# Kernel tuning notes

Hardware: AMD Instinct MI355X
Metric: run time of the kernel (lower is better)

The kernel has to match this reference:

```python
import jax, jax.numpy as jnp
import numpy as np

B, N, DIM, DEPTH, H, DH, MLP = 8, 1024, 768, 6, 12, 64, 3072
INNER = H * DH
LN_EPS = 1e-5


def setup_inputs() -> dict:
    key = jax.random.key(0)
    ks = jax.random.split(key, 8)
    return {
        "x": jax.random.normal(ks[0], (B, N, DIM), jnp.float32),
        "ln1_g": jnp.ones((DEPTH, DIM), jnp.float32),
        "ln1_b": jnp.zeros((DEPTH, DIM), jnp.float32),
        "Wq": jax.random.normal(ks[1], (DEPTH, DIM, INNER), jnp.float32) * 0.02,
        "Wkv": jax.random.normal(ks[2], (DEPTH, DIM, 2 * INNER), jnp.float32) * 0.02,
        "mix_pre": jax.random.normal(ks[3], (DEPTH, H, H), jnp.float32),
        "mix_post": jax.random.normal(ks[4], (DEPTH, H, H), jnp.float32),
        "Wo": jax.random.normal(ks[5], (DEPTH, INNER, DIM), jnp.float32) * 0.02,
        "bo": jnp.zeros((DEPTH, DIM), jnp.float32),
        "s1": jnp.full((DEPTH, DIM), 0.1, jnp.float32),  # LayerScale init_eps for depth<=18
        "ln2_g": jnp.ones((DEPTH, DIM), jnp.float32),
        "ln2_b": jnp.zeros((DEPTH, DIM), jnp.float32),
        "W1": jax.random.normal(ks[6], (DEPTH, DIM, MLP), jnp.float32) * 0.02,
        "b1": jnp.zeros((DEPTH, MLP), jnp.float32),
        "W2": jax.random.normal(ks[7], (DEPTH, MLP, DIM), jnp.float32) * 0.02,
        "b2": jnp.zeros((DEPTH, DIM), jnp.float32),
        "s2": jnp.full((DEPTH, DIM), 0.1, jnp.float32),
    }


def _ln(x, g, b):
    m = jnp.mean(x, axis=-1, keepdims=True)
    v = jnp.mean(jnp.square(x - m), axis=-1, keepdims=True)
    return (x - m) * jax.lax.rsqrt(v + LN_EPS) * g + b


def reference(x, ln1_g, ln1_b, Wq, Wkv, mix_pre, mix_post, Wo, bo, s1,
              ln2_g, ln2_b, W1, b1, W2, b2, s2):
    depth = Wq.shape[0]
    heads = mix_pre.shape[-1]
    dim_head = Wq.shape[-1] // heads
    scale = dim_head ** -0.5
    b_, n_ = x.shape[0], x.shape[1]

    def split_heads(t):  # [b, n, h*d] -> [b, h, n, d]
        return t.reshape(b_, n_, heads, dim_head).transpose(0, 2, 1, 3)

    for i in range(depth):
        # --- talking-heads attention block (PreNorm + LayerScale) ---
        h = _ln(x, ln1_g[i], ln1_b[i])
        q = split_heads(h @ Wq[i])
        kv = h @ Wkv[i]
        k = split_heads(kv[..., : heads * dim_head])
        v = split_heads(kv[..., heads * dim_head:])
        dots = jnp.einsum('bhid,bhjd->bhij', q, k) * scale
        dots = jnp.einsum('bhij,hg->bgij', dots, mix_pre[i])  # pre-softmax head mix
        attn = jax.nn.softmax(dots, axis=-1)
        attn = jnp.einsum('bhij,hg->bgij', attn, mix_post[i])  # post-softmax head mix
        out = jnp.einsum('bhij,bhjd->bhid', attn, v)
        out = out.transpose(0, 2, 1, 3).reshape(b_, n_, heads * dim_head)
        x = (out @ Wo[i] + bo[i]) * s1[i] + x
        # --- feed-forward block (PreNorm + LayerScale) ---
        h = _ln(x, ln2_g[i], ln2_b[i])
        h = jax.nn.gelu(h @ W1[i] + b1[i], approximate=False) @ W2[i] + b2[i]
        x = h * s2[i] + x
    return x
```

## Files before the change

kernel.cpp:

```cpp
#include <hip/hip_runtime.h>

constexpr int kDepth = 6;
constexpr int kB = 8;
constexpr int kN = 1024;
constexpr int kDim = 768;
constexpr int kH = 12;
constexpr int kDh = 64;
constexpr int kMlp = 3072;
constexpr int kRows = kB * kN;
constexpr int kQKV = 2304;

typedef __attribute__((ext_vector_type(4))) float f32x4;
typedef __attribute__((ext_vector_type(8))) short bf16x8;

__device__ __forceinline__ f32x4 mfma16x16x32(bf16x8 a, bf16x8 b, f32x4 c) {
  return __builtin_amdgcn_mfma_f32_16x16x32_bf16(a, b, c, 0, 0, 0);
}

__device__ __forceinline__ unsigned short f2bf(float f) {
  unsigned int u = __builtin_bit_cast(unsigned int, f);
  u = u + 0x7FFFu + ((u >> 16) & 1u);
  return (unsigned short)(u >> 16);
}

__device__ __forceinline__ float bf2f(unsigned short u) {
  return __builtin_bit_cast(float, (unsigned int)u << 16);
}

__device__ __forceinline__ void gload_lds16(const void* g, void* l) {
  __builtin_amdgcn_global_load_lds((__attribute__((address_space(1))) void*)g,
                                   (__attribute__((address_space(3))) void*)l,
                                   16, 0, 0);
}

__global__ __launch_bounds__(256) void ln_kernel(const float* __restrict__ x,
                                                 const float* __restrict__ gamma,
                                                 const float* __restrict__ beta,
                                                 unsigned short* __restrict__ out) {
  int row = blockIdx.x, tid = threadIdx.x;
  const float* xr = x + (size_t)row * kDim;
  float v0 = xr[tid], v1 = xr[tid + 256], v2 = xr[tid + 512];
  float s = v0 + v1 + v2;
  float q = v0 * v0 + v1 * v1 + v2 * v2;
#pragma unroll
  for (int o = 32; o >= 1; o >>= 1) {
    s += __shfl_xor(s, o);
    q += __shfl_xor(q, o);
  }
  __shared__ float ss[4], sq[4];
  int wid = tid >> 6, lane = tid & 63;
  if (lane == 0) { ss[wid] = s; sq[wid] = q; }
  __syncthreads();
  s = ss[0] + ss[1] + ss[2] + ss[3];
  q = sq[0] + sq[1] + sq[2] + sq[3];
  float mean = s * (1.0f / kDim);
  float var = q * (1.0f / kDim) - mean * mean;
  float rstd = rsqrtf(var + 1e-5f);
  unsigned short* orow = out + (size_t)row * kDim;
  orow[tid]       = f2bf((v0 - mean) * rstd * gamma[tid]       + beta[tid]);
  orow[tid + 256] = f2bf((v1 - mean) * rstd * gamma[tid + 256] + beta[tid + 256]);
  orow[tid + 512] = f2bf((v2 - mean) * rstd * gamma[tid + 512] + beta[tid + 512]);
}

__global__ __launch_bounds__(256) void transpose_all(const float* __restrict__ Wq,
                                                     const float* __restrict__ Wkv,
                                                     const float* __restrict__ Wo,
                                                     const float* __restrict__ W1,
                                                     const float* __restrict__ W2,
                                                     unsigned short* __restrict__ wqkvT,
                                                     unsigned short* __restrict__ woT,
                                                     unsigned short* __restrict__ w1T,
                                                     unsigned short* __restrict__ w2T,
                                                     int L) {
  int t = blockIdx.x;
  const float* src;
  unsigned short* dst;
  int R, C, dstOff;
  if (t < 576)       { src = Wq  + (size_t)L * 768 * 768;  R = 768;  C = 768;  dst = wqkvT; dstOff = 0;   }
  else if (t < 1728) { src = Wkv + (size_t)L * 768 * 1536; R = 768;  C = 1536; dst = wqkvT; dstOff = 768; t -= 576; }
  else if (t < 2304) { src = Wo  + (size_t)L * 768 * 768;  R = 768;  C = 768;  dst = woT;   dstOff = 0;   t -= 1728; }
  else if (t < 4608) { src = W1  + (size_t)L * 768 * 3072; R = 768;  C = 3072; dst = w1T;   dstOff = 0;   t -= 2304; }
  else               { src = W2  + (size_t)L * 3072 * 768; R = 3072; C = 768;  dst = w2T;   dstOff = 0;   t -= 4608; }
  int Ct = C >> 5;
  int bx = t % Ct, by = t / Ct;
  __shared__ float tt[32][33];
  int tx = threadIdx.x & 31, ty = threadIdx.x >> 5;
  int c0 = bx * 32, r0 = by * 32;
#pragma unroll
  for (int k = 0; k < 4; ++k) {
    int r = r0 + ty + k * 8;
    tt[ty + k * 8][tx] = src[(size_t)r * C + c0 + tx];
  }
  __syncthreads();
#pragma unroll
  for (int k = 0; k < 4; ++k) {
    int c = c0 + ty + k * 8;
    dst[(size_t)(dstOff + c) * R + r0 + tx] = f2bf(tt[tx][ty + k * 8]);
  }
}

__global__ __launch_bounds__(256) void transpose_v_kernel(const unsigned short* __restrict__ qkv,
                                                          unsigned short* __restrict__ vT) {
  __shared__ unsigned short t[32][33];
  int tx = threadIdx.x & 31, ty = threadIdx.x >> 5;
  int j0 = blockIdx.x * 32, d0 = blockIdx.y * 32;
  int bg = blockIdx.z;
  int b = bg / kH, g = bg % kH;
#pragma unroll
  for (int k = 0; k < 4; ++k) {
    int j = j0 + ty + k * 8;
    t[ty + k * 8][tx] = qkv[(size_t)(b * kN + j) * kQKV + 1536 + g * 64 + d0 + tx];
  }
  __syncthreads();
#pragma unroll
  for (int k = 0; k < 4; ++k) {
    int d = d0 + ty + k * 8;
    vT[((size_t)(b * kH + g) * kDh + d) * kN + j0 + tx] = t[tx][ty + k * 8];
  }
}

template <int EPI>
__global__ __launch_bounds__(256) void gemm_kernel(const unsigned short* __restrict__ A,
                                                   const unsigned short* __restrict__ Bt,
                                                   const float* __restrict__ bias,
                                                   const float* __restrict__ scl,
                                                   float* __restrict__ resid,
                                                   unsigned short* __restrict__ C,
                                                   int K, int ldc) {
  __shared__ __align__(16) unsigned short lA[128 * 64];
  __shared__ __align__(16) unsigned short lB[128 * 64];
  int tid = threadIdx.x, wid = tid >> 6, lane = tid & 63;
  int gx = gridDim.x;
  int nwg = gx * gridDim.y;
  int orig = blockIdx.y * gx + blockIdx.x;
  int chunk = nwg >> 3;
  int wg = (orig & 7) * chunk + (orig >> 3);
  int bx = wg % gx, by = wg / gx;
  int row0 = by * 128, col0 = bx * 128;
  int wr = wid >> 1, wc = wid & 1;
  f32x4 zero = {0.f, 0.f, 0.f, 0.f};
  f32x4 acc[4][4];
#pragma unroll
  for (int m = 0; m < 4; ++m)
#pragma unroll
    for (int n = 0; n < 4; ++n) acc[m][n] = zero;

  for (int kt = 0; kt < K; kt += 64) {
    __syncthreads();
#pragma unroll
    for (int t = 0; t < 4; ++t) {
      int cbase = wid * 256 + t * 64;
      int c = cbase + lane;
      int r = c >> 3, slot = c & 7;
      int k8 = slot ^ (r & 7);
      gload_lds16(&A[(size_t)(row0 + r) * K + kt + k8 * 8], &lA[cbase * 8]);
      gload_lds16(&Bt[(size_t)(col0 + r) * K + kt + k8 * 8], &lB[cbase * 8]);
    }
    __syncthreads();
#pragma unroll
    for (int kk = 0; kk < 2; ++kk) {
      bf16x8 af[4], bfr[4];
      int kslot = kk * 4 + (lane >> 4);
#pragma unroll
      for (int m = 0; m < 4; ++m) {
        int r = wr * 64 + m * 16 + (lane & 15);
        af[m] = *reinterpret_cast<const bf16x8*>(&lA[r * 64 + ((kslot ^ (r & 7)) << 3)]);
      }
#pragma unroll
      for (int n = 0; n < 4; ++n) {
        int r = wc * 64 + n * 16 + (lane & 15);
        bfr[n] = *reinterpret_cast<const bf16x8*>(&lB[r * 64 + ((kslot ^ (r & 7)) << 3)]);
      }
#pragma unroll
      for (int m = 0; m < 4; ++m)
#pragma unroll
        for (int n = 0; n < 4; ++n) acc[m][n] = mfma16x16x32(af[m], bfr[n], acc[m][n]);
    }
  }
#pragma unroll
  for (int m = 0; m < 4; ++m)
#pragma unroll
    for (int n = 0; n < 4; ++n)
#pragma unroll
      for (int r4 = 0; r4 < 4; ++r4) {
        int row = row0 + wr * 64 + m * 16 + ((lane >> 4) << 2) + r4;
        int col = col0 + wc * 64 + n * 16 + (lane & 15);
        float v = acc[m][n][r4];
        if (EPI == 0) {
          C[(size_t)row * ldc + col] = f2bf(v);
        } else if (EPI == 1) {
          v += bias[col];
          v = 0.5f * v * (1.f + erff(v * 0.70710678118654752f));
          C[(size_t)row * ldc + col] = f2bf(v);
        } else {
          v = (v + bias[col]) * scl[col];
          size_t idx = (size_t)row * kDim + col;
          resid[idx] = resid[idx] + v;
        }
      }
}

__global__ __launch_bounds__(256) void dots_kernel(const unsigned short* __restrict__ qkv,
                                                   unsigned short* __restrict__ dots,
                                                   int i0, int IC) {
  constexpr int TROW = 24;
  __shared__ __align__(16) unsigned short T[32 * 32 * TROW];
  int tid = threadIdx.x, wid = tid >> 6, lane = tid & 63;
  int kg = lane >> 4, l15 = lane & 15;
  int j0 = blockIdx.x * 32;
  int il0 = blockIdx.y * 32;
  int b = blockIdx.z;
  for (int idx = tid; idx < 2048; idx += 256) {
    int pos = idx >> 1;
    *(unsigned int*)&T[pos * TROW + 12 + (idx & 1) * 2] = 0u;
  }
  f32x4 zero = {0.f, 0.f, 0.f, 0.f};
#pragma unroll
  for (int rep = 0; rep < 3; ++rep) {
    int h = rep * 4 + wid;
    f32x4 acc[2][2];
    acc[0][0] = zero; acc[0][1] = zero; acc[1][0] = zero; acc[1][1] = zero;
#pragma unroll
    for (int kk = 0; kk < 2; ++kk) {
      bf16x8 aq[2], bk[2];
#pragma unroll
      for (int m = 0; m < 2; ++m) {
        int tok = i0 + il0 + m * 16 + l15;
        aq[m] = *reinterpret_cast<const bf16x8*>(
            &qkv[(size_t)(b * kN + tok) * kQKV + h * 64 + kk * 32 + kg * 8]);
      }
#pragma unroll
      for (int n = 0; n < 2; ++n) {
        int tj = j0 + n * 16 + l15;
        bk[n] = *reinterpret_cast<const bf16x8*>(
            &qkv[(size_t)(b * kN + tj) * kQKV + 768 + h * 64 + kk * 32 + kg * 8]);
      }
#pragma unroll
      for (int m = 0; m < 2; ++m)
#pragma unroll
        for (int n = 0; n < 2; ++n) acc[m][n] = mfma16x16x32(aq[m], bk[n], acc[m][n]);
    }
#pragma unroll
    for (int m = 0; m < 2; ++m)
#pragma unroll
      for (int n = 0; n < 2; ++n)
#pragma unroll
        for (int r = 0; r < 4; ++r)
          T[((m * 16 + kg * 4 + r) * 32 + n * 16 + l15) * TROW + h] = f2bf(acc[m][n][r]);
  }
  __syncthreads();
#pragma unroll
  for (int k = 0; k < 8; ++k) {
    int c = tid + k * 256;
    int pos = c >> 1, half = c & 1;
    int ii = pos >> 5, jj = pos & 31;
    *(f32x4*)&dots[((size_t)(b * IC + il0 + ii) * kN + j0 + jj) * 16 + half * 8] =
        *(const f32x4*)&T[pos * TROW + half * 8];
  }
}

__global__ __launch_bounds__(256) void softmax_mix_kernel(const unsigned short* __restrict__ dots,
                                                          const float* __restrict__ pre,
                                                          const float* __restrict__ post,
                                                          unsigned short* __restrict__ pbuf,
                                                          int IC) {
  constexpr int EROW = 24;
  __shared__ __align__(16) unsigned short E[1024 * EROW];
  __shared__ __align__(16) unsigned short preA[16 * 32];
  __shared__ __align__(16) unsigned short postA[16 * 32];
  __shared__ float red[4][16];
  __shared__ float lgs[16];
  int tid = threadIdx.x, wid = tid >> 6, lane = tid & 63;
  int kg = lane >> 4, l15 = lane & 15;
  int i = blockIdx.x, b = blockIdx.y;
  for (int idx = tid; idx < 512; idx += 256) {
    int m = idx >> 5, k = idx & 31;
    preA[idx] = f2bf((m < 12 && k < 12) ? pre[k * 12 + m] * 0.125f : 0.f);
  }
  __syncthreads();
  bf16x8 preF = *(const bf16x8*)&preA[l15 * 32 + kg * 8];
  const unsigned short* drow = dots + (size_t)(b * IC + i) * kN * 16;
  f32x4 zero = {0.f, 0.f, 0.f, 0.f};
  bf16x8 zfrag = {0, 0, 0, 0, 0, 0, 0, 0};
  float psum[4] = {0.f, 0.f, 0.f, 0.f};
#pragma unroll
  for (int grp = 0; grp < 16; ++grp) {
    int j = wid * 256 + grp * 16 + l15;
    bf16x8 bfrag = (kg < 2) ? *(const bf16x8*)&drow[(size_t)j * 16 + kg * 8] : zfrag;
    f32x4 d = mfma16x16x32(preF, bfrag, zero);
    float ee[4];
#pragma unroll
    for (int r = 0; r < 4; ++r) {
      float dc = fminf(fmaxf(d[r], -15.f), 15.f);
      ee[r] = (kg == 3) ? 0.f : __expf(dc);
      psum[r] += ee[r];
    }
    unsigned int w0, w1;
    asm("v_cvt_pk_bf16_f32 %0, %1, %2" : "=v"(w0) : "v"(ee[0]), "v"(ee[1]));
    asm("v_cvt_pk_bf16_f32 %0, %1, %2" : "=v"(w1) : "v"(ee[2]), "v"(ee[3]));
    *(unsigned int*)&E[j * EROW + kg * 4] = w0;
    *(unsigned int*)&E[j * EROW + kg * 4 + 2] = w1;
  }
#pragma unroll
  for (int r = 0; r < 4; ++r) {
    psum[r] += __shfl_xor(psum[r], 1);
    psum[r] += __shfl_xor(psum[r], 2);
    psum[r] += __shfl_xor(psum[r], 4);
    psum[r] += __shfl_xor(psum[r], 8);
  }
  if (l15 == 0) {
#pragma unroll
    for (int r = 0; r < 4; ++r) red[wid][kg * 4 + r] = psum[r];
  }
  __syncthreads();
  if (tid < 16) {
    float s = red[0][tid] + red[1][tid] + red[2][tid] + red[3][tid];
    lgs[tid] = (tid < 12) ? 1.f / s : 0.f;
  }
  __syncthreads();
  for (int idx = tid; idx < 512; idx += 256) {
    int m = idx >> 5, k = idx & 31;
    postA[idx] = f2bf((m < 12 && k < 12) ? post[k * 12 + m] * lgs[k] : 0.f);
  }
  __syncthreads();
  bf16x8 postF = *(const bf16x8*)&postA[l15 * 32 + kg * 8];
#pragma unroll
  for (int grp = 0; grp < 16; ++grp) {
    int j = wid * 256 + grp * 16 + l15;
    bf16x8 efrag = (kg < 2) ? *(const bf16x8*)&E[j * EROW + kg * 8] : zfrag;
    f32x4 d2 = mfma16x16x32(postF, efrag, zero);
    if (kg < 3) {
#pragma unroll
      for (int r = 0; r < 4; ++r) {
        int g2 = kg * 4 + r;
        pbuf[((size_t)(b * kH + g2) * IC + i) * kN + j] = f2bf(d2[r]);
      }
    }
  }
}

__global__ __launch_bounds__(256) void pv_kernel(const unsigned short* __restrict__ pbuf,
                                                 const unsigned short* __restrict__ vT,
                                                 unsigned short* __restrict__ attn_out,
                                                 int i0, int IC) {
  int tid = threadIdx.x, wid = tid >> 6, lane = tid & 63;
  int kg = lane >> 4, l15 = lane & 15;
  int i32 = blockIdx.x * 32;
  int g = blockIdx.y, b = blockIdx.z;
  const unsigned short* prow = pbuf + (size_t)(b * kH + g) * IC * kN;
  const unsigned short* vrow = vT + (size_t)(b * kH + g) * kDh * kN;
  f32x4 zero = {0.f, 0.f, 0.f, 0.f};
  f32x4 acc[2][4];
#pragma unroll
  for (int half = 0; half < 2; ++half)
#pragma unroll
    for (int n = 0; n < 4; ++n) acc[half][n] = zero;
#pragma unroll
  for (int s = 0; s < 8; ++s) {
    int kt = (wid * 8 + s) * 32 + kg * 8;
    bf16x8 ap[2];
#pragma unroll
    for (int half = 0; half < 2; ++half)
      ap[half] = *reinterpret_cast<const bf16x8*>(&prow[(size_t)(i32 + half * 16 + l15) * kN + kt]);
#pragma unroll
    for (int n = 0; n < 4; ++n) {
      bf16x8 bv = *reinterpret_cast<const bf16x8*>(&vrow[(size_t)(n * 16 + l15) * kN + kt]);
#pragma unroll
      for (int half = 0; half < 2; ++half)
        acc[half][n] = mfma16x16x32(ap[half], bv, acc[half][n]);
    }
  }
  __shared__ float red[3][32][64];
  if (wid > 0) {
#pragma unroll
    for (int half = 0; half < 2; ++half)
#pragma unroll
      for (int n = 0; n < 4; ++n)
#pragma unroll
        for (int r = 0; r < 4; ++r)
          red[wid - 1][half * 16 + kg * 4 + r][n * 16 + l15] = acc[half][n][r];
  }
  __syncthreads();
  if (wid == 0) {
#pragma unroll
    for (int half = 0; half < 2; ++half)
#pragma unroll
      for (int n = 0; n < 4; ++n)
#pragma unroll
        for (int r = 0; r < 4; ++r) {
          int rr = half * 16 + kg * 4 + r, cc = n * 16 + l15;
          float v = acc[half][n][r] + red[0][rr][cc] + red[1][rr][cc] + red[2][rr][cc];
          int tok = i0 + i32 + rr;
          attn_out[(size_t)(b * kN + tok) * kDim + g * kDh + cc] = f2bf(v);
        }
  }
}

extern "C" void kernel_launch(void* const* d_in, const int* in_sizes, int n_in,
                              void* d_out, int out_size, void* d_ws, size_t ws_size,
                              hipStream_t stream) {
  (void)in_sizes; (void)n_in; (void)out_size;
  const float* x     = (const float*)d_in[0];
  const float* ln1_g = (const float*)d_in[1];
  const float* ln1_b = (const float*)d_in[2];
  const float* Wq    = (const float*)d_in[3];
  const float* Wkv   = (const float*)d_in[4];
  const float* pre   = (const float*)d_in[5];
  const float* post  = (const float*)d_in[6];
  const float* Wo    = (const float*)d_in[7];
  const float* bo    = (const float*)d_in[8];
  const float* s1    = (const float*)d_in[9];
  const float* ln2_g = (const float*)d_in[10];
  const float* ln2_b = (const float*)d_in[11];
  const float* W1    = (const float*)d_in[12];
  const float* b1    = (const float*)d_in[13];
  const float* W2    = (const float*)d_in[14];
  const float* b2    = (const float*)d_in[15];
  const float* s2    = (const float*)d_in[16];
  float* xo = (float*)d_out;

  char* ws = (char*)d_ws;
  size_t off = 0;
  auto alloc = [&](size_t bytes) -> void* {
    void* p = ws + off;
    off += (bytes + 255) & ~(size_t)255;
    return p;
  };
  unsigned short* h_buf   = (unsigned short*)alloc((size_t)kRows * kDim * 2);
  unsigned short* qkv     = (unsigned short*)alloc((size_t)kRows * kQKV * 2);
  unsigned short* vT      = (unsigned short*)alloc((size_t)kB * kH * kDh * kN * 2);
  unsigned short* attnout = (unsigned short*)alloc((size_t)kRows * kDim * 2);
  unsigned short* mid     = (unsigned short*)alloc((size_t)kRows * kMlp * 2);
  unsigned short* wqkvT   = (unsigned short*)alloc((size_t)kQKV * kDim * 2);
  unsigned short* woT     = (unsigned short*)alloc((size_t)kDim * kDim * 2);
  unsigned short* w1T     = (unsigned short*)alloc((size_t)kMlp * kDim * 2);
  unsigned short* w2T     = (unsigned short*)alloc((size_t)kDim * kMlp * 2);

  size_t base = off;
  int IC = 1024;
  while (IC > 32 && base + (size_t)IC * (262144 + 196608) + 1024 > ws_size) IC >>= 1;
  unsigned short* dots = (unsigned short*)alloc((size_t)kB * IC * kN * 16 * 2);
  unsigned short* pbuf = (unsigned short*)alloc((size_t)kB * kH * IC * kN * 2);

  hipMemcpyAsync(xo, x, (size_t)kRows * kDim * 4, hipMemcpyDeviceToDevice, stream);

  for (int L = 0; L < kDepth; ++L) {
    ln_kernel<<<kRows, 256, 0, stream>>>(xo, ln1_g + L * kDim, ln1_b + L * kDim, h_buf);
    transpose_all<<<6912, 256, 0, stream>>>(Wq, Wkv, Wo, W1, W2, wqkvT, woT, w1T, w2T, L);

    gemm_kernel<0><<<dim3(kQKV / 128, kRows / 128), 256, 0, stream>>>(
        h_buf, wqkvT, nullptr, nullptr, nullptr, qkv, kDim, kQKV);
    transpose_v_kernel<<<dim3(kN / 32, kDh / 32, kB * kH), 256, 0, stream>>>(qkv, vT);

    for (int i0 = 0; i0 < kN; i0 += IC) {
      dots_kernel<<<dim3(kN / 32, IC / 32, kB), 256, 0, stream>>>(qkv, dots, i0, IC);
      softmax_mix_kernel<<<dim3(IC, kB), 256, 0, stream>>>(
          dots, pre + L * 144, post + L * 144, pbuf, IC);
      pv_kernel<<<dim3(IC / 32, kH, kB), 256, 0, stream>>>(pbuf, vT, attnout, i0, IC);
    }
    gemm_kernel<2><<<dim3(kDim / 128, kRows / 128), 256, 0, stream>>>(
        attnout, woT, bo + L * kDim, s1 + L * kDim, xo, nullptr, kDim, kDim);

    ln_kernel<<<kRows, 256, 0, stream>>>(xo, ln2_g + L * kDim, ln2_b + L * kDim, h_buf);
    gemm_kernel<1><<<dim3(kMlp / 128, kRows / 128), 256, 0, stream>>>(
        h_buf, w1T, b1 + L * kMlp, nullptr, nullptr, mid, kDim, kMlp);
    gemm_kernel<2><<<dim3(kDim / 128, kRows / 128), 256, 0, stream>>>(
        mid, w2T, b2 + L * kDim, s2 + L * kDim, xo, nullptr, kMlp, kDim);
  }
}
```

Before: 3.528 ms.

## Fuse QK^T, talking-heads softmax and PV into one two-pass attention kernel

Replaces the dots, softmax_mix and pv kernels with a single kernel per 32-query block that never writes the dots or probability tensors to global memory. A first pass recomputes QK^T tiles in LDS and applies the pre-mix to accumulate softmax denominators in registers. A second pass recomputes the tiles, normalizes, applies the post-mix and accumulates P·V directly. This removes large intermediate global buffers and the query chunking, at the cost of computing QK^T twice and launching only 256 blocks with heavy per-tile synchronization, so the GPU may run at low occupancy.

```diff
diff --git a/kernel.cpp b/kernel.cpp
--- a/kernel.cpp
+++ b/kernel.cpp
@@ -200,206 +200,186 @@
       }
 }
 
-__global__ __launch_bounds__(256) void dots_kernel(const unsigned short* __restrict__ qkv,
-                                                   unsigned short* __restrict__ dots,
-                                                   int i0, int IC) {
+__global__ __launch_bounds__(256) void fused_attn_kernel(
+    const unsigned short* __restrict__ qkv,
+    const float* __restrict__ pre, const float* __restrict__ post,
+    const unsigned short* __restrict__ vT,
+    unsigned short* __restrict__ attnout) {
   constexpr int TROW = 24;
-  __shared__ __align__(16) unsigned short T[32 * 32 * TROW];
+  constexpr int P2ROW = 40;
+  __shared__ __align__(16) unsigned short T[1024 * TROW];
+  __shared__ __align__(16) unsigned short P2[12 * 32 * P2ROW];
+  __shared__ __align__(16) unsigned short preA[16 * 32];
+  __shared__ __align__(16) unsigned short postA[16 * 32];
   int tid = threadIdx.x, wid = tid >> 6, lane = tid & 63;
   int kg = lane >> 4, l15 = lane & 15;
-  int j0 = blockIdx.x * 32;
-  int il0 = blockIdx.y * 32;
-  int b = blockIdx.z;
+  int it0 = blockIdx.x * 32;
+  int b = blockIdx.y;
+
+  for (int idx = tid; idx < 512; idx += 256) {
+    int m = idx >> 5, k = idx & 31;
+    bool in = (m < 12 && k < 12);
+    preA[idx]  = f2bf(in ? pre[k * 12 + m] * 0.125f : 0.f);
+    postA[idx] = f2bf(in ? post[k * 12 + m] : 0.f);
+  }
   for (int idx = tid; idx < 2048; idx += 256) {
     int pos = idx >> 1;
     *(unsigned int*)&T[pos * TROW + 12 + (idx & 1) * 2] = 0u;
   }
-  f32x4 zero = {0.f, 0.f, 0.f, 0.f};
-#pragma unroll
-  for (int rep = 0; rep < 3; ++rep) {
-    int h = rep * 4 + wid;
-    f32x4 acc[2][2];
-    acc[0][0] = zero; acc[0][1] = zero; acc[1][0] = zero; acc[1][1] = zero;
-#pragma unroll
-    for (int kk = 0; kk < 2; ++kk) {
-      bf16x8 aq[2], bk[2];
-#pragma unroll
-      for (int m = 0; m < 2; ++m) {
-        int tok = i0 + il0 + m * 16 + l15;
-        aq[m] = *reinterpret_cast<const bf16x8*>(
-            &qkv[(size_t)(b * kN + tok) * kQKV + h * 64 + kk * 32 + kg * 8]);
-      }
-#pragma unroll
-      for (int n = 0; n < 2; ++n) {
-        int tj = j0 + n * 16 + l15;
-        bk[n] = *reinterpret_cast<const bf16x8*>(
-            &qkv[(size_t)(b * kN + tj) * kQKV + 768 + h * 64 + kk * 32 + kg * 8]);
-      }
-#pragma unroll
-      for (int m = 0; m < 2; ++m)
-#pragma unroll
-        for (int n = 0; n < 2; ++n) acc[m][n] = mfma16x16x32(aq[m], bk[n], acc[m][n]);
-    }
-#pragma unroll
-    for (int m = 0; m < 2; ++m)
-#pragma unroll
-      for (int n = 0; n < 2; ++n)
-#pragma unroll
-        for (int r = 0; r < 4; ++r)
-          T[((m * 16 + kg * 4 + r) * 32 + n * 16 + l15) * TROW + h] = f2bf(acc[m][n][r]);
-  }
   __syncthreads();
-#pragma unroll
-  for (int k = 0; k < 8; ++k) {
-    int c = tid + k * 256;
-    int pos = c >> 1, half = c & 1;
-    int ii = pos >> 5, jj = pos & 31;
-    *(f32x4*)&dots[((size_t)(b * IC + il0 + ii) * kN + j0 + jj) * 16 + half * 8] =
-        *(const f32x4*)&T[pos * TROW + half * 8];
-  }
-}
-
-__global__ __launch_bounds__(256) void softmax_mix_kernel(const unsigned short* __restrict__ dots,
-                                                          const float* __restrict__ pre,
-                                                          const float* __restrict__ post,
-                                                          unsigned short* __restrict__ pbuf,
-                                                          int IC) {
-  constexpr int EROW = 24;
-  __shared__ __align__(16) unsigned short E[1024 * EROW];
-  __shared__ __align__(16) unsigned short preA[16 * 32];
-  __shared__ __align__(16) unsigned short postA[16 * 32];
-  __shared__ float red[4][16];
-  __shared__ float lgs[16];
-  int tid = threadIdx.x, wid = tid >> 6, lane = tid & 63;
-  int kg = lane >> 4, l15 = lane & 15;
-  int i = blockIdx.x, b = blockIdx.y;
-  for (int idx = tid; idx < 512; idx += 256) {
-    int m = idx >> 5, k = idx & 31;
-    preA[idx] = f2bf((m < 12 && k < 12) ? pre[k * 12 + m] * 0.125f : 0.f);
-  }
-  __syncthreads();
-  bf16x8 preF = *(const bf16x8*)&preA[l15 * 32 + kg * 8];
-  const unsigned short* drow = dots + (size_t)(b * IC + i) * kN * 16;
+  bf16x8 preF  = *(const bf16x8*)&preA[l15 * 32 + kg * 8];
+  bf16x8 postF = *(const bf16x8*)&postA[l15 * 32 + kg * 8];
   f32x4 zero = {0.f, 0.f, 0.f, 0.f};
   bf16x8 zfrag = {0, 0, 0, 0, 0, 0, 0, 0};
-  float psum[4] = {0.f, 0.f, 0.f, 0.f};
-#pragma unroll
-  for (int grp = 0; grp < 16; ++grp) {
-    int j = wid * 256 + grp * 16 + l15;
-    bf16x8 bfrag = (kg < 2) ? *(const bf16x8*)&drow[(size_t)j * 16 + kg * 8] : zfrag;
-    f32x4 d = mfma16x16x32(preF, bfrag, zero);
-    float ee[4];
+
+  auto qkt_tile = [&](int j0) {
+#pragma unroll
+    for (int rep = 0; rep < 3; ++rep) {
+      int h = rep * 4 + wid;
+      f32x4 acc2[2][2];
+      acc2[0][0] = zero; acc2[0][1] = zero; acc2[1][0] = zero; acc2[1][1] = zero;
+#pragma unroll
+      for (int kk = 0; kk < 2; ++kk) {
+        bf16x8 aq[2], bk[2];
+#pragma unroll
+        for (int m = 0; m < 2; ++m)
+          aq[m] = *(const bf16x8*)&qkv[(size_t)(b * kN + it0 + m * 16 + l15) * kQKV +
+                                       h * 64 + kk * 32 + kg * 8];
+#pragma unroll
+        for (int n = 0; n < 2; ++n)
+          bk[n] = *(const bf16x8*)&qkv[(size_t)(b * kN + j0 + n * 16 + l15) * kQKV +
+                                       768 + h * 64 + kk * 32 + kg * 8];
+#pragma unroll
+        for (int m = 0; m < 2; ++m)
+#pragma unroll
+          for (int n = 0; n < 2; ++n) acc2[m][n] = mfma16x16x32(aq[m], bk[n], acc2[m][n]);
+      }
+#pragma unroll
+      for (int m = 0; m < 2; ++m)
+#pragma unroll
+        for (int n = 0; n < 2; ++n)
+#pragma unroll
+          for (int r = 0; r < 4; ++r)
+            T[((m * 16 + kg * 4 + r) * 32 + n * 16 + l15) * TROW + h] = f2bf(acc2[m][n][r]);
+    }
+  };
+
+  float psum[8][4];
+#pragma unroll
+  for (int il = 0; il < 8; ++il)
+#pragma unroll
+    for (int r = 0; r < 4; ++r) psum[il][r] = 0.f;
+
+  for (int t = 0; t < 32; ++t) {
+    __syncthreads();
+    qkt_tile(t * 32);
+    __syncthreads();
+#pragma unroll
+    for (int grp = 0; grp < 16; ++grp) {
+      int pos = wid * 256 + grp * 16 + l15;
+      bf16x8 bfrag = (kg < 2) ? *(const bf16x8*)&T[pos * TROW + kg * 8] : zfrag;
+      f32x4 d = mfma16x16x32(preF, bfrag, zero);
+#pragma unroll
+      for (int r = 0; r < 4; ++r) {
+        float dc = fminf(fmaxf(d[r], -15.f), 15.f);
+        float ee = (kg == 3) ? 0.f : __expf(dc);
+        psum[grp >> 1][r] += ee;
+      }
+    }
+  }
+  float lgr[8][4];
+#pragma unroll
+  for (int il = 0; il < 8; ++il)
 #pragma unroll
     for (int r = 0; r < 4; ++r) {
-      float dc = fminf(fmaxf(d[r], -15.f), 15.f);
-      ee[r] = (kg == 3) ? 0.f : __expf(dc);
-      psum[r] += ee[r];
-    }
-    unsigned int w0, w1;
-    asm("v_cvt_pk_bf16_f32 %0, %1, %2" : "=v"(w0) : "v"(ee[0]), "v"(ee[1]));
-    asm("v_cvt_pk_bf16_f32 %0, %1, %2" : "=v"(w1) : "v"(ee[2]), "v"(ee[3]));
-    *(unsigned int*)&E[j * EROW + kg * 4] = w0;
-    *(unsigned int*)&E[j * EROW + kg * 4 + 2] = w1;
-  }
-#pragma unroll
-  for (int r = 0; r < 4; ++r) {
-    psum[r] += __shfl_xor(psum[r], 1);
-    psum[r] += __shfl_xor(psum[r], 2);
-    psum[r] += __shfl_xor(psum[r], 4);
-    psum[r] += __shfl_xor(psum[r], 8);
-  }
-  if (l15 == 0) {
-#pragma unroll
-    for (int r = 0; r < 4; ++r) red[wid][kg * 4 + r] = psum[r];
-  }
-  __syncthreads();
-  if (tid < 16) {
-    float s = red[0][tid] + red[1][tid] + red[2][tid] + red[3][tid];
-    lgs[tid] = (tid < 12) ? 1.f / s : 0.f;
-  }
-  __syncthreads();
-  for (int idx = tid; idx < 512; idx += 256) {
-    int m = idx >> 5, k = idx & 31;
-    postA[idx] = f2bf((m < 12 && k < 12) ? post[k * 12 + m] * lgs[k] : 0.f);
-  }
-  __syncthreads();
-  bf16x8 postF = *(const bf16x8*)&postA[l15 * 32 + kg * 8];
-#pragma unroll
-  for (int grp = 0; grp < 16; ++grp) {
-    int j = wid * 256 + grp * 16 + l15;
-    bf16x8 efrag = (kg < 2) ? *(const bf16x8*)&E[j * EROW + kg * 8] : zfrag;
-    f32x4 d2 = mfma16x16x32(postF, efrag, zero);
-    if (kg < 3) {
+      float s = psum[il][r];
+      s += __shfl_xor(s, 1); s += __shfl_xor(s, 2);
+      s += __shfl_xor(s, 4); s += __shfl_xor(s, 8);
+      lgr[il][r] = (kg < 3) ? (1.f / s) : 0.f;
+    }
+
+  f32x4 pvacc[3][2][4];
+#pragma unroll
+  for (int gg = 0; gg < 3; ++gg)
+#pragma unroll
+    for (int hh = 0; hh < 2; ++hh)
+#pragma unroll
+      for (int n = 0; n < 4; ++n) pvacc[gg][hh][n] = zero;
+  int g2w = wid * 3;
+
+  for (int t = 0; t < 32; ++t) {
+    int j0 = t * 32;
+    __syncthreads();
+    qkt_tile(j0);
+    __syncthreads();
+#pragma unroll
+    for (int grp = 0; grp < 16; ++grp) {
+      int pos = wid * 256 + grp * 16 + l15;
+      bf16x8 bfrag = (kg < 2) ? *(const bf16x8*)&T[pos * TROW + kg * 8] : zfrag;
+      f32x4 d = mfma16x16x32(preF, bfrag, zero);
+      float pe[4];
 #pragma unroll
       for (int r = 0; r < 4; ++r) {
-        int g2 = kg * 4 + r;
-        pbuf[((size_t)(b * kH + g2) * IC + i) * kN + j] = f2bf(d2[r]);
-      }
-    }
-  }
-}
-
-__global__ __launch_bounds__(256) void pv_kernel(const unsigned short* __restrict__ pbuf,
-                                                 const unsigned short* __restrict__ vT,
-                                                 unsigned short* __restrict__ attn_out,
-                                                 int i0, int IC) {
-  int tid = threadIdx.x, wid = tid >> 6, lane = tid & 63;
-  int kg = lane >> 4, l15 = lane & 15;
-  int i32 = blockIdx.x * 32;
-  int g = blockIdx.y, b = blockIdx.z;
-  const unsigned short* prow = pbuf + (size_t)(b * kH + g) * IC * kN;
-  const unsigned short* vrow = vT + (size_t)(b * kH + g) * kDh * kN;
-  f32x4 zero = {0.f, 0.f, 0.f, 0.f};
-  f32x4 acc[2][4];
-#pragma unroll
-  for (int half = 0; half < 2; ++half)
-#pragma unroll
-    for (int n = 0; n < 4; ++n) acc[half][n] = zero;
-#pragma unroll
-  for (int s = 0; s < 8; ++s) {
-    int kt = (wid * 8 + s) * 32 + kg * 8;
-    bf16x8 ap[2];
-#pragma unroll
-    for (int half = 0; half < 2; ++half)
-      ap[half] = *reinterpret_cast<const bf16x8*>(&prow[(size_t)(i32 + half * 16 + l15) * kN + kt]);
-#pragma unroll
-    for (int n = 0; n < 4; ++n) {
-      bf16x8 bv = *reinterpret_cast<const bf16x8*>(&vrow[(size_t)(n * 16 + l15) * kN + kt]);
-#pragma unroll
-      for (int half = 0; half < 2; ++half)
-        acc[half][n] = mfma16x16x32(ap[half], bv, acc[half][n]);
-    }
-  }
-  __shared__ float red[3][32][64];
-  if (wid > 0) {
-#pragma unroll
-    for (int half = 0; half < 2; ++half)
+        float dc = fminf(fmaxf(d[r], -15.f), 15.f);
+        float ee = (kg == 3) ? 0.f : __expf(dc);
+        pe[r] = ee * lgr[grp >> 1][r];
+      }
+      unsigned int w0, w1;
+      asm("v_cvt_pk_bf16_f32 %0, %1, %2" : "=v"(w0) : "v"(pe[0]), "v"(pe[1]));
+      asm("v_cvt_pk_bf16_f32 %0, %1, %2" : "=v"(w1) : "v"(pe[2]), "v"(pe[3]));
+      *(unsigned int*)&T[pos * TROW + kg * 4] = w0;
+      *(unsigned int*)&T[pos * TROW + kg * 4 + 2] = w1;
+    }
+    __syncthreads();
+#pragma unroll
+    for (int grp = 0; grp < 16; ++grp) {
+      int pos = wid * 256 + grp * 16 + l15;
+      bf16x8 efrag = (kg < 2) ? *(const bf16x8*)&T[pos * TROW + kg * 8] : zfrag;
+      f32x4 d2 = mfma16x16x32(postF, efrag, zero);
+      if (kg < 3) {
+        int ii = wid * 8 + (grp >> 1);
+        int jj = (grp & 1) * 16 + l15;
+#pragma unroll
+        for (int r = 0; r < 4; ++r)
+          P2[((kg * 4 + r) * 32 + ii) * P2ROW + jj] = f2bf(d2[r]);
+      }
+    }
+    __syncthreads();
+#pragma unroll
+    for (int gg = 0; gg < 3; ++gg) {
+      int g2 = g2w + gg;
+      bf16x8 ap[2];
+#pragma unroll
+      for (int hh = 0; hh < 2; ++hh)
+        ap[hh] = *(const bf16x8*)&P2[((size_t)g2 * 32 + hh * 16 + l15) * P2ROW + kg * 8];
+#pragma unroll
+      for (int n = 0; n < 4; ++n) {
+        bf16x8 bv = *(const bf16x8*)&vT[((size_t)(b * 12 + g2) * 64 + n * 16 + l15) * kN +
+                                        j0 + kg * 8];
+#pragma unroll
+        for (int hh = 0; hh < 2; ++hh)
+          pvacc[gg][hh][n] = mfma16x16x32(ap[hh], bv, pvacc[gg][hh][n]);
+      }
+    }
+  }
+#pragma unroll
+  for (int gg = 0; gg < 3; ++gg)
+#pragma unroll
+    for (int hh = 0; hh < 2; ++hh)
 #pragma unroll
       for (int n = 0; n < 4; ++n)
 #pragma unroll
-        for (int r = 0; r < 4; ++r)
-          red[wid - 1][half * 16 + kg * 4 + r][n * 16 + l15] = acc[half][n][r];
-  }
-  __syncthreads();
-  if (wid == 0) {
-#pragma unroll
-    for (int half = 0; half < 2; ++half)
-#pragma unroll
-      for (int n = 0; n < 4; ++n)
-#pragma unroll
         for (int r = 0; r < 4; ++r) {
-          int rr = half * 16 + kg * 4 + r, cc = n * 16 + l15;
-          float v = acc[half][n][r] + red[0][rr][cc] + red[1][rr][cc] + red[2][rr][cc];
-          int tok = i0 + i32 + rr;
-          attn_out[(size_t)(b * kN + tok) * kDim + g * kDh + cc] = f2bf(v);
+          int tok = it0 + hh * 16 + kg * 4 + r;
+          int col = (g2w + gg) * 64 + n * 16 + l15;
+          attnout[(size_t)(b * kN + tok) * kDim + col] = f2bf(pvacc[gg][hh][n][r]);
         }
-  }
 }
 
 extern "C" void kernel_launch(void* const* d_in, const int* in_sizes, int n_in,
                               void* d_out, int out_size, void* d_ws, size_t ws_size,
                               hipStream_t stream) {
-  (void)in_sizes; (void)n_in; (void)out_size;
+  (void)in_sizes; (void)n_in; (void)out_size; (void)ws_size;
   const float* x     = (const float*)d_in[0];
   const float* ln1_g = (const float*)d_in[1];
   const float* ln1_b = (const float*)d_in[2];
@@ -436,12 +416,6 @@
   unsigned short* w1T     = (unsigned short*)alloc((size_t)kMlp * kDim * 2);
   unsigned short* w2T     = (unsigned short*)alloc((size_t)kDim * kMlp * 2);
 
-  size_t base = off;
-  int IC = 1024;
-  while (IC > 32 && base + (size_t)IC * (262144 + 196608) + 1024 > ws_size) IC >>= 1;
-  unsigned short* dots = (unsigned short*)alloc((size_t)kB * IC * kN * 16 * 2);
-  unsigned short* pbuf = (unsigned short*)alloc((size_t)kB * kH * IC * kN * 2);
-
   hipMemcpyAsync(xo, x, (size_t)kRows * kDim * 4, hipMemcpyDeviceToDevice, stream);
 
   for (int L = 0; L < kDepth; ++L) {
@@ -452,12 +426,9 @@
         h_buf, wqkvT, nullptr, nullptr, nullptr, qkv, kDim, kQKV);
     transpose_v_kernel<<<dim3(kN / 32, kDh / 32, kB * kH), 256, 0, stream>>>(qkv, vT);
 
-    for (int i0 = 0; i0 < kN; i0 += IC) {
-      dots_kernel<<<dim3(kN / 32, IC / 32, kB), 256, 0, stream>>>(qkv, dots, i0, IC);
-      softmax_mix_kernel<<<dim3(IC, kB), 256, 0, stream>>>(
-          dots, pre + L * 144, post + L * 144, pbuf, IC);
-      pv_kernel<<<dim3(IC / 32, kH, kB), 256, 0, stream>>>(pbuf, vT, attnout, i0, IC);
-    }
+    fused_attn_kernel<<<dim3(kN / 32, kB), 256, 0, stream>>>(
+        qkv, pre + L * 144, post + L * 144, vT, attnout);
+
     gemm_kernel<2><<<dim3(kDim / 128, kRows / 128), 256, 0, stream>>>(
         attnout, woT, bo + L * kDim, s1 + L * kDim, xo, nullptr, kDim, kDim);
 
```

After: 3.721 ms. +5.5%, slower.

## Fuse softmax-mix with PV into one kernel and split-K the W2 GEMM

Applied to the files above, without the earlier changes.

Merges the softmax/post-mix kernel and the PV kernel into a single kernel. It recomputes the pre-mix logits in two passes, first for the row sums and then to produce normalized probabilities, and keeps the post-mixed probabilities in LDS for an immediate MFMA against V^T. This removes the large pbuf write and read round trip and frees its workspace, so the query chunk can be bigger. It also splits the K=3072 FFN-down GEMM into two halves along a grid z dimension, which doubles its block count and accumulates into the residual with atomicAdd. The cost is recomputing the exp work twice, extra barriers per tile, a grid for the fused kernel that may be small, and nondeterministic fp32 atomic summation.

```diff
diff --git a/kernel.cpp b/kernel.cpp
--- a/kernel.cpp
+++ b/kernel.cpp
@@ -126,7 +126,7 @@
                                                    const float* __restrict__ scl,
                                                    float* __restrict__ resid,
                                                    unsigned short* __restrict__ C,
-                                                   int K, int ldc) {
+                                                   int K, int ldc, int lda) {
   __shared__ __align__(16) unsigned short lA[128 * 64];
   __shared__ __align__(16) unsigned short lB[128 * 64];
   int tid = threadIdx.x, wid = tid >> 6, lane = tid & 63;
@@ -137,6 +137,7 @@
   int wg = (orig & 7) * chunk + (orig >> 3);
   int bx = wg % gx, by = wg / gx;
   int row0 = by * 128, col0 = bx * 128;
+  int koff = (EPI == 3) ? blockIdx.z * K : 0;
   int wr = wid >> 1, wc = wid & 1;
   f32x4 zero = {0.f, 0.f, 0.f, 0.f};
   f32x4 acc[4][4];
@@ -153,8 +154,8 @@
       int c = cbase + lane;
       int r = c >> 3, slot = c & 7;
       int k8 = slot ^ (r & 7);
-      gload_lds16(&A[(size_t)(row0 + r) * K + kt + k8 * 8], &lA[cbase * 8]);
-      gload_lds16(&Bt[(size_t)(col0 + r) * K + kt + k8 * 8], &lB[cbase * 8]);
+      gload_lds16(&A[(size_t)(row0 + r) * lda + koff + kt + k8 * 8], &lA[cbase * 8]);
+      gload_lds16(&Bt[(size_t)(col0 + r) * lda + koff + kt + k8 * 8], &lB[cbase * 8]);
     }
     __syncthreads();
 #pragma unroll
@@ -192,10 +193,14 @@
           v += bias[col];
           v = 0.5f * v * (1.f + erff(v * 0.70710678118654752f));
           C[(size_t)row * ldc + col] = f2bf(v);
-        } else {
+        } else if (EPI == 2) {
           v = (v + bias[col]) * scl[col];
           size_t idx = (size_t)row * kDim + col;
           resid[idx] = resid[idx] + v;
+        } else {
+          if (blockIdx.z == 0) v += bias[col];
+          v *= scl[col];
+          atomicAdd(&resid[(size_t)row * kDim + col], v);
         }
       }
 }
@@ -259,141 +264,134 @@
   }
 }
 
-__global__ __launch_bounds__(256) void softmax_mix_kernel(const unsigned short* __restrict__ dots,
-                                                          const float* __restrict__ pre,
-                                                          const float* __restrict__ post,
-                                                          unsigned short* __restrict__ pbuf,
-                                                          int IC) {
-  constexpr int EROW = 24;
-  __shared__ __align__(16) unsigned short E[1024 * EROW];
+__global__ __launch_bounds__(256) void softmax_pv_kernel(
+    const unsigned short* __restrict__ dots,
+    const float* __restrict__ pre, const float* __restrict__ post,
+    const unsigned short* __restrict__ vT,
+    unsigned short* __restrict__ attnout, int i0, int IC) {
+  constexpr int EROW = 40;
+  constexpr int PROW = 40;
+  __shared__ __align__(16) unsigned short E[512 * EROW];
+  __shared__ __align__(16) unsigned short P2[192 * PROW];
   __shared__ __align__(16) unsigned short preA[16 * 32];
   __shared__ __align__(16) unsigned short postA[16 * 32];
-  __shared__ float red[4][16];
-  __shared__ float lgs[16];
   int tid = threadIdx.x, wid = tid >> 6, lane = tid & 63;
   int kg = lane >> 4, l15 = lane & 15;
-  int i = blockIdx.x, b = blockIdx.y;
+  int itl = blockIdx.x * 16;
+  int b = blockIdx.y;
+
   for (int idx = tid; idx < 512; idx += 256) {
     int m = idx >> 5, k = idx & 31;
-    preA[idx] = f2bf((m < 12 && k < 12) ? pre[k * 12 + m] * 0.125f : 0.f);
+    bool in = (m < 12 && k < 12);
+    preA[idx]  = f2bf(in ? pre[k * 12 + m] * 0.125f : 0.f);
+    postA[idx] = f2bf(in ? post[k * 12 + m] : 0.f);
   }
   __syncthreads();
-  bf16x8 preF = *(const bf16x8*)&preA[l15 * 32 + kg * 8];
-  const unsigned short* drow = dots + (size_t)(b * IC + i) * kN * 16;
+  bf16x8 preF  = *(const bf16x8*)&preA[l15 * 32 + kg * 8];
+  bf16x8 postF = *(const bf16x8*)&postA[l15 * 32 + kg * 8];
   f32x4 zero = {0.f, 0.f, 0.f, 0.f};
   bf16x8 zfrag = {0, 0, 0, 0, 0, 0, 0, 0};
-  float psum[4] = {0.f, 0.f, 0.f, 0.f};
-#pragma unroll
-  for (int grp = 0; grp < 16; ++grp) {
-    int j = wid * 256 + grp * 16 + l15;
-    bf16x8 bfrag = (kg < 2) ? *(const bf16x8*)&drow[(size_t)j * 16 + kg * 8] : zfrag;
-    f32x4 d = mfma16x16x32(preF, bfrag, zero);
-    float ee[4];
+  const unsigned short* dbase = dots + (size_t)b * IC * kN * 16;
+
+  float psum[4][4];
+#pragma unroll
+  for (int a = 0; a < 4; ++a)
+#pragma unroll
+    for (int r = 0; r < 4; ++r) psum[a][r] = 0.f;
+#pragma unroll
+  for (int a = 0; a < 4; ++a) {
+    const unsigned short* dr = dbase + (size_t)(itl + wid * 4 + a) * kN * 16;
+    for (int jg = 0; jg < 64; ++jg) {
+      bf16x8 bfrag = (kg < 2) ? *(const bf16x8*)&dr[(jg * 16 + l15) * 16 + kg * 8] : zfrag;
+      f32x4 d = mfma16x16x32(preF, bfrag, zero);
+#pragma unroll
+      for (int r = 0; r < 4; ++r) {
+        float dc = fminf(fmaxf(d[r], -15.f), 15.f);
+        psum[a][r] += (kg == 3) ? 0.f : __expf(dc);
+      }
+    }
+  }
+  float lgr[4][4];
+#pragma unroll
+  for (int a = 0; a < 4; ++a)
 #pragma unroll
     for (int r = 0; r < 4; ++r) {
-      float dc = fminf(fmaxf(d[r], -15.f), 15.f);
-      ee[r] = (kg == 3) ? 0.f : __expf(dc);
-      psum[r] += ee[r];
-    }
-    unsigned int w0, w1;
-    asm("v_cvt_pk_bf16_f32 %0, %1, %2" : "=v"(w0) : "v"(ee[0]), "v"(ee[1]));
-    asm("v_cvt_pk_bf16_f32 %0, %1, %2" : "=v"(w1) : "v"(ee[2]), "v"(ee[3]));
-    *(unsigned int*)&E[j * EROW + kg * 4] = w0;
-    *(unsigned int*)&E[j * EROW + kg * 4 + 2] = w1;
-  }
-#pragma unroll
-  for (int r = 0; r < 4; ++r) {
-    psum[r] += __shfl_xor(psum[r], 1);
-    psum[r] += __shfl_xor(psum[r], 2);
-    psum[r] += __shfl_xor(psum[r], 4);
-    psum[r] += __shfl_xor(psum[r], 8);
-  }
-  if (l15 == 0) {
-#pragma unroll
-    for (int r = 0; r < 4; ++r) red[wid][kg * 4 + r] = psum[r];
-  }
-  __syncthreads();
-  if (tid < 16) {
-    float s = red[0][tid] + red[1][tid] + red[2][tid] + red[3][tid];
-    lgs[tid] = (tid < 12) ? 1.f / s : 0.f;
-  }
-  __syncthreads();
-  for (int idx = tid; idx < 512; idx += 256) {
-    int m = idx >> 5, k = idx & 31;
-    postA[idx] = f2bf((m < 12 && k < 12) ? post[k * 12 + m] * lgs[k] : 0.f);
-  }
-  __syncthreads();
-  bf16x8 postF = *(const bf16x8*)&postA[l15 * 32 + kg * 8];
-#pragma unroll
-  for (int grp = 0; grp < 16; ++grp) {
-    int j = wid * 256 + grp * 16 + l15;
-    bf16x8 efrag = (kg < 2) ? *(const bf16x8*)&E[j * EROW + kg * 8] : zfrag;
-    f32x4 d2 = mfma16x16x32(postF, efrag, zero);
-    if (kg < 3) {
+      float s = psum[a][r];
+      s += __shfl_xor(s, 1); s += __shfl_xor(s, 2);
+      s += __shfl_xor(s, 4); s += __shfl_xor(s, 8);
+      lgr[a][r] = (kg < 3) ? (1.f / s) : 0.f;
+    }
+
+  f32x4 pvacc[3][4];
+#pragma unroll
+  for (int gg = 0; gg < 3; ++gg)
+#pragma unroll
+    for (int n = 0; n < 4; ++n) pvacc[gg][n] = zero;
+  int g2w = wid * 3;
+
+  for (int t = 0; t < 32; ++t) {
+    int j0 = t * 32;
+#pragma unroll
+    for (int a = 0; a < 4; ++a) {
+      int ir = wid * 4 + a;
+      const unsigned short* dr = dbase + (size_t)(itl + ir) * kN * 16;
+#pragma unroll
+      for (int jh = 0; jh < 2; ++jh) {
+        bf16x8 bfrag = (kg < 2) ? *(const bf16x8*)&dr[(j0 + jh * 16 + l15) * 16 + kg * 8] : zfrag;
+        f32x4 d = mfma16x16x32(preF, bfrag, zero);
+        float pe[4];
+#pragma unroll
+        for (int r = 0; r < 4; ++r) {
+          float dc = fminf(fmaxf(d[r], -15.f), 15.f);
+          float ee = (kg == 3) ? 0.f : __expf(dc);
+          pe[r] = ee * lgr[a][r];
+        }
+        unsigned int w0, w1;
+        asm("v_cvt_pk_bf16_f32 %0, %1, %2" : "=v"(w0) : "v"(pe[0]), "v"(pe[1]));
+        asm("v_cvt_pk_bf16_f32 %0, %1, %2" : "=v"(w1) : "v"(pe[2]), "v"(pe[3]));
+        int pos = ir * 32 + jh * 16 + l15;
+        *(unsigned int*)&E[pos * EROW + kg * 4] = w0;
+        *(unsigned int*)&E[pos * EROW + kg * 4 + 2] = w1;
+      }
+    }
+    __syncthreads();
+#pragma unroll
+    for (int pp = 0; pp < 8; ++pp) {
+      int p = wid * 8 + pp;
+      bf16x8 ef = (kg < 2) ? *(const bf16x8*)&E[(p * 16 + l15) * EROW + kg * 8] : zfrag;
+      f32x4 d2 = mfma16x16x32(postF, ef, zero);
+      if (kg < 3) {
+        int pos = p * 16 + l15;
+        int ir = pos >> 5, jj = pos & 31;
+#pragma unroll
+        for (int r = 0; r < 4; ++r)
+          P2[((kg * 4 + r) * 16 + ir) * PROW + jj] = f2bf(d2[r]);
+      }
+    }
+    __syncthreads();
+#pragma unroll
+    for (int gg = 0; gg < 3; ++gg) {
+      int g2 = g2w + gg;
+      bf16x8 ap = *(const bf16x8*)&P2[(g2 * 16 + l15) * PROW + kg * 8];
+#pragma unroll
+      for (int n = 0; n < 4; ++n) {
+        bf16x8 bv = *(const bf16x8*)&vT[((size_t)(b * kH + g2) * kDh + n * 16 + l15) * kN +
+                                        j0 + kg * 8];
+        pvacc[gg][n] = mfma16x16x32(ap, bv, pvacc[gg][n]);
+      }
+    }
+    __syncthreads();
+  }
+#pragma unroll
+  for (int gg = 0; gg < 3; ++gg)
+#pragma unroll
+    for (int n = 0; n < 4; ++n)
 #pragma unroll
       for (int r = 0; r < 4; ++r) {
-        int g2 = kg * 4 + r;
-        pbuf[((size_t)(b * kH + g2) * IC + i) * kN + j] = f2bf(d2[r]);
-      }
-    }
-  }
-}
-
-__global__ __launch_bounds__(256) void pv_kernel(const unsigned short* __restrict__ pbuf,
-                                                 const unsigned short* __restrict__ vT,
-                                                 unsigned short* __restrict__ attn_out,
-                                                 int i0, int IC) {
-  int tid = threadIdx.x, wid = tid >> 6, lane = tid & 63;
-  int kg = lane >> 4, l15 = lane & 15;
-  int i32 = blockIdx.x * 32;
-  int g = blockIdx.y, b = blockIdx.z;
-  const unsigned short* prow = pbuf + (size_t)(b * kH + g) * IC * kN;
-  const unsigned short* vrow = vT + (size_t)(b * kH + g) * kDh * kN;
-  f32x4 zero = {0.f, 0.f, 0.f, 0.f};
-  f32x4 acc[2][4];
-#pragma unroll
-  for (int half = 0; half < 2; ++half)
-#pragma unroll
-    for (int n = 0; n < 4; ++n) acc[half][n] = zero;
-#pragma unroll
-  for (int s = 0; s < 8; ++s) {
-    int kt = (wid * 8 + s) * 32 + kg * 8;
-    bf16x8 ap[2];
-#pragma unroll
-    for (int half = 0; half < 2; ++half)
-      ap[half] = *reinterpret_cast<const bf16x8*>(&prow[(size_t)(i32 + half * 16 + l15) * kN + kt]);
-#pragma unroll
-    for (int n = 0; n < 4; ++n) {
-      bf16x8 bv = *reinterpret_cast<const bf16x8*>(&vrow[(size_t)(n * 16 + l15) * kN + kt]);
-#pragma unroll
-      for (int half = 0; half < 2; ++half)
-        acc[half][n] = mfma16x16x32(ap[half], bv, acc[half][n]);
-    }
-  }
-  __shared__ float red[3][32][64];
-  if (wid > 0) {
-#pragma unroll
-    for (int half = 0; half < 2; ++half)
-#pragma unroll
-      for (int n = 0; n < 4; ++n)
-#pragma unroll
-        for (int r = 0; r < 4; ++r)
-          red[wid - 1][half * 16 + kg * 4 + r][n * 16 + l15] = acc[half][n][r];
-  }
-  __syncthreads();
-  if (wid == 0) {
-#pragma unroll
-    for (int half = 0; half < 2; ++half)
-#pragma unroll
-      for (int n = 0; n < 4; ++n)
-#pragma unroll
-        for (int r = 0; r < 4; ++r) {
-          int rr = half * 16 + kg * 4 + r, cc = n * 16 + l15;
-          float v = acc[half][n][r] + red[0][rr][cc] + red[1][rr][cc] + red[2][rr][cc];
-          int tok = i0 + i32 + rr;
-          attn_out[(size_t)(b * kN + tok) * kDim + g * kDh + cc] = f2bf(v);
-        }
-  }
+        int tok = i0 + itl + kg * 4 + r;
+        int col = (g2w + gg) * 64 + n * 16 + l15;
+        attnout[(size_t)(b * kN + tok) * kDim + col] = f2bf(pvacc[gg][n][r]);
+      }
 }
 
 extern "C" void kernel_launch(void* const* d_in, const int* in_sizes, int n_in,
@@ -438,9 +436,8 @@
 
   size_t base = off;
   int IC = 1024;
-  while (IC > 32 && base + (size_t)IC * (262144 + 196608) + 1024 > ws_size) IC >>= 1;
+  while (IC > 32 && base + (size_t)IC * 262144 + 1024 > ws_size) IC >>= 1;
   unsigned short* dots = (unsigned short*)alloc((size_t)kB * IC * kN * 16 * 2);
-  unsigned short* pbuf = (unsigned short*)alloc((size_t)kB * kH * IC * kN * 2);
 
   hipMemcpyAsync(xo, x, (size_t)kRows * kDim * 4, hipMemcpyDeviceToDevice, stream);
 
@@ -449,22 +446,21 @@
     transpose_all<<<6912, 256, 0, stream>>>(Wq, Wkv, Wo, W1, W2, wqkvT, woT, w1T, w2T, L);
 
     gemm_kernel<0><<<dim3(kQKV / 128, kRows / 128), 256, 0, stream>>>(
-        h_buf, wqkvT, nullptr, nullptr, nullptr, qkv, kDim, kQKV);
+        h_buf, wqkvT, nullptr, nullptr, nullptr, qkv, kDim, kQKV, kDim);
     transpose_v_kernel<<<dim3(kN / 32, kDh / 32, kB * kH), 256, 0, stream>>>(qkv, vT);
 
     for (int i0 = 0; i0 < kN; i0 += IC) {
       dots_kernel<<<dim3(kN / 32, IC / 32, kB), 256, 0, stream>>>(qkv, dots, i0, IC);
-      softmax_mix_kernel<<<dim3(IC, kB), 256, 0, stream>>>(
-          dots, pre + L * 144, post + L * 144, pbuf, IC);
-      pv_kernel<<<dim3(IC / 32, kH, kB), 256, 0, stream>>>(pbuf, vT, attnout, i0, IC);
+      softmax_pv_kernel<<<dim3(IC / 16, kB), 256, 0, stream>>>(
+          dots, pre + L * 144, post + L * 144, vT, attnout, i0, IC);
     }
     gemm_kernel<2><<<dim3(kDim / 128, kRows / 128), 256, 0, stream>>>(
-        attnout, woT, bo + L * kDim, s1 + L * kDim, xo, nullptr, kDim, kDim);
+        attnout, woT, bo + L * kDim, s1 + L * kDim, xo, nullptr, kDim, kDim, kDim);
 
     ln_kernel<<<kRows, 256, 0, stream>>>(xo, ln2_g + L * kDim, ln2_b + L * kDim, h_buf);
     gemm_kernel<1><<<dim3(kMlp / 128, kRows / 128), 256, 0, stream>>>(
-        h_buf, w1T, b1 + L * kMlp, nullptr, nullptr, mid, kDim, kMlp);
-    gemm_kernel<2><<<dim3(kDim / 128, kRows / 128), 256, 0, stream>>>(
-        mid, w2T, b2 + L * kDim, s2 + L * kDim, xo, nullptr, kMlp, kDim);
-  }
-}
+        h_buf, w1T, b1 + L * kMlp, nullptr, nullptr, mid, kDim, kMlp, kDim);
+    gemm_kernel<3><<<dim3(kDim / 128, kRows / 128, 2), 256, 0, stream>>>(
+        mid, w2T, b2 + L * kDim, s2 + L * kDim, xo, nullptr, kMlp / 2, kDim, kMlp);
+  }
+}
```

Result: slower. 8.093 ms (+129.4%).

## Split the W2 MLP GEMM along K into two halves with a reduction kernel

Applied to the files above, without the earlier changes.

The down-projection GEMM (K=3072, only 6x64 output tiles) is launched with a z-dimension of 2. Each half writes fp32 partial sums to a new workspace buffer, and a separate reduce kernel adds bias, LayerScale and the residual. The aim is more blocks per launch, to reduce wave-quantization and tail underutilisation on the GPU's compute units. In exchange it adds about 50 MB of extra fp32 partial writes and reads, plus one more kernel launch per layer.

```diff
diff --git a/kernel.cpp b/kernel.cpp
--- a/kernel.cpp
+++ b/kernel.cpp
@@ -126,7 +126,7 @@
                                                    const float* __restrict__ scl,
                                                    float* __restrict__ resid,
                                                    unsigned short* __restrict__ C,
-                                                   int K, int ldc) {
+                                                   int K, int ldc, int lda) {
   __shared__ __align__(16) unsigned short lA[128 * 64];
   __shared__ __align__(16) unsigned short lB[128 * 64];
   int tid = threadIdx.x, wid = tid >> 6, lane = tid & 63;
@@ -137,6 +137,7 @@
   int wg = (orig & 7) * chunk + (orig >> 3);
   int bx = wg % gx, by = wg / gx;
   int row0 = by * 128, col0 = bx * 128;
+  int koff = (EPI == 3) ? blockIdx.z * K : 0;
   int wr = wid >> 1, wc = wid & 1;
   f32x4 zero = {0.f, 0.f, 0.f, 0.f};
   f32x4 acc[4][4];
@@ -153,8 +154,8 @@
       int c = cbase + lane;
       int r = c >> 3, slot = c & 7;
       int k8 = slot ^ (r & 7);
-      gload_lds16(&A[(size_t)(row0 + r) * K + kt + k8 * 8], &lA[cbase * 8]);
-      gload_lds16(&Bt[(size_t)(col0 + r) * K + kt + k8 * 8], &lB[cbase * 8]);
+      gload_lds16(&A[(size_t)(row0 + r) * lda + koff + kt + k8 * 8], &lA[cbase * 8]);
+      gload_lds16(&Bt[(size_t)(col0 + r) * lda + koff + kt + k8 * 8], &lB[cbase * 8]);
     }
     __syncthreads();
 #pragma unroll
@@ -192,12 +193,29 @@
           v += bias[col];
           v = 0.5f * v * (1.f + erff(v * 0.70710678118654752f));
           C[(size_t)row * ldc + col] = f2bf(v);
-        } else {
+        } else if (EPI == 2) {
           v = (v + bias[col]) * scl[col];
           size_t idx = (size_t)row * kDim + col;
           resid[idx] = resid[idx] + v;
+        } else {
+          resid[(size_t)blockIdx.z * kRows * kDim + (size_t)row * kDim + col] = v;
         }
       }
+}
+
+__global__ __launch_bounds__(256) void reduce_w2(const float* __restrict__ pw,
+                                                 const float* __restrict__ bias,
+                                                 const float* __restrict__ scl,
+                                                 float* __restrict__ xo) {
+  int row = blockIdx.x, tid = threadIdx.x;
+  const float* p0 = pw + (size_t)row * kDim;
+  const float* p1 = pw + (size_t)kRows * kDim + (size_t)row * kDim;
+  float* xr = xo + (size_t)row * kDim;
+#pragma unroll
+  for (int k = 0; k < 3; ++k) {
+    int c = tid + k * 256;
+    xr[c] = xr[c] + (p0[c] + p1[c] + bias[c]) * scl[c];
+  }
 }
 
 __global__ __launch_bounds__(256) void dots_kernel(const unsigned short* __restrict__ qkv,
@@ -435,6 +453,7 @@
   unsigned short* woT     = (unsigned short*)alloc((size_t)kDim * kDim * 2);
   unsigned short* w1T     = (unsigned short*)alloc((size_t)kMlp * kDim * 2);
   unsigned short* w2T     = (unsigned short*)alloc((size_t)kDim * kMlp * 2);
+  float* pw               = (float*)alloc((size_t)2 * kRows * kDim * 4);
 
   size_t base = off;
   int IC = 1024;
@@ -449,7 +468,7 @@
     transpose_all<<<6912, 256, 0, stream>>>(Wq, Wkv, Wo, W1, W2, wqkvT, woT, w1T, w2T, L);
 
     gemm_kernel<0><<<dim3(kQKV / 128, kRows / 128), 256, 0, stream>>>(
-        h_buf, wqkvT, nullptr, nullptr, nullptr, qkv, kDim, kQKV);
+        h_buf, wqkvT, nullptr, nullptr, nullptr, qkv, kDim, kQKV, kDim);
     transpose_v_kernel<<<dim3(kN / 32, kDh / 32, kB * kH), 256, 0, stream>>>(qkv, vT);
 
     for (int i0 = 0; i0 < kN; i0 += IC) {
@@ -459,12 +478,13 @@
       pv_kernel<<<dim3(IC / 32, kH, kB), 256, 0, stream>>>(pbuf, vT, attnout, i0, IC);
     }
     gemm_kernel<2><<<dim3(kDim / 128, kRows / 128), 256, 0, stream>>>(
-        attnout, woT, bo + L * kDim, s1 + L * kDim, xo, nullptr, kDim, kDim);
+        attnout, woT, bo + L * kDim, s1 + L * kDim, xo, nullptr, kDim, kDim, kDim);
 
     ln_kernel<<<kRows, 256, 0, stream>>>(xo, ln2_g + L * kDim, ln2_b + L * kDim, h_buf);
     gemm_kernel<1><<<dim3(kMlp / 128, kRows / 128), 256, 0, stream>>>(
-        h_buf, w1T, b1 + L * kMlp, nullptr, nullptr, mid, kDim, kMlp);
-    gemm_kernel<2><<<dim3(kDim / 128, kRows / 128), 256, 0, stream>>>(
-        mid, w2T, b2 + L * kDim, s2 + L * kDim, xo, nullptr, kMlp, kDim);
-  }
-}
+        h_buf, w1T, b1 + L * kMlp, nullptr, nullptr, mid, kDim, kMlp, kDim);
+    gemm_kernel<3><<<dim3(kDim / 128, kRows / 128, 2), 256, 0, stream>>>(
+        mid, w2T, nullptr, nullptr, pw, nullptr, kMlp / 2, kDim, kMlp);
+    reduce_w2<<<kRows, 256, 0, stream>>>(pw, b2 + L * kDim, s2 + L * kDim, xo);
+  }
+}
```

Measured after the change: 3.995 ms. 1.13x slower.
